# Optimization experiments

Measured on AMD Instinct MI355X. Metric: run time of the kernel, lower is better.

## Reference

```python
import jax, jax.numpy as jnp
import numpy as np

INPUT_SIZE = 256
HIDDEN_SIZE = 512
OUTPUT_SIZE = 256
SEQ_LEN = 32768


def setup_inputs() -> dict:
    key = jax.random.key(0)
    k_x, k_wx, k_wh, k_wy = jax.random.split(key, 4)
    x = jax.random.normal(k_x, (SEQ_LEN, INPUT_SIZE), dtype=jnp.float32)
    Wx = jax.random.normal(k_wx, (HIDDEN_SIZE, INPUT_SIZE), dtype=jnp.float32) * np.sqrt(2.0 / (INPUT_SIZE + HIDDEN_SIZE))
    Wh = jax.random.normal(k_wh, (HIDDEN_SIZE, HIDDEN_SIZE), dtype=jnp.float32) * np.sqrt(1.0 / HIDDEN_SIZE)
    Wy = jax.random.normal(k_wy, (OUTPUT_SIZE, HIDDEN_SIZE), dtype=jnp.float32) * np.sqrt(2.0 / (HIDDEN_SIZE + OUTPUT_SIZE))
    bh = jnp.zeros((HIDDEN_SIZE, 1), dtype=jnp.float32)
    by = jnp.zeros((OUTPUT_SIZE, 1), dtype=jnp.float32)
    return {"x": x, "Wx": Wx, "Wh": Wh, "Wy": Wy, "bh": bh, "by": by}


def reference(x, Wx, Wh, Wy, bh, by):
    # x: [T, I]; Wx: [H, I]; Wh: [H, H]; Wy: [O, H]; bh: [H,1]; by: [O,1]
    bh_v = bh[:, 0]  # [H]
    by_v = by[:, 0]  # [O]
    h0 = jnp.zeros((Wh.shape[0],), dtype=x.dtype)

    def step(h, x_t):
        # h_t = tanh(Wx @ x_t + Wh @ h_{t-1} + bh)
        h_new = jnp.tanh(Wx @ x_t + Wh @ h + bh_v)
        return h_new, h_new

    _, h_hist = jax.lax.scan(step, h0, x)  # [T, H]
    # y_t = Wy @ h_t + by, concatenated and flattened -> [T * O]
    y = h_hist @ Wy.T + by_v  # [T, O]
    return y.reshape(-1)
```

## Files before the change

kernel.cpp:

```cpp
#include <hip/hip_runtime.h>

#define SEQ 32768
#define ISZ 256
#define HSZ 512
#define OSZ 256
#define NLAUNCH 64
#define RTHREADS 512
#define SENT 0x7FAAAAAAu
#define KFAST 8
#define LATCH_T 48

typedef unsigned long long u64;
typedef _Float16 half2_t __attribute__((ext_vector_type(2)));

#if defined(__has_builtin)
#if __has_builtin(__builtin_amdgcn_fdot2)
#define HAVE_FDOT2 1
#endif
#endif

__device__ __forceinline__ float dot2f(half2_t a, half2_t b, float c) {
#ifdef HAVE_FDOT2
  return __builtin_amdgcn_fdot2(a, b, c, false);
#else
  return fmaf((float)a.x, (float)b.x, fmaf((float)a.y, (float)b.y, c));
#endif
}
__device__ __forceinline__ half2_t bch2(unsigned u) {
  return __builtin_bit_cast(half2_t, u);
}
__device__ __forceinline__ unsigned pkrtz_u(float x, float y) {
  return __builtin_bit_cast(unsigned, __builtin_amdgcn_cvt_pkrtz(x, y));
}

__global__ __launch_bounds__(256) void gemm_bt_bias(
    const float* __restrict__ A, const float* __restrict__ W,
    const float* __restrict__ bias, float* __restrict__ C,
    int M, int N, int K)
{
  __shared__ float As[32][68];
  __shared__ float Bs[32][68];
  const int tx = threadIdx.x;
  const int tn = tx & 15, tm = tx >> 4;
  const int m0 = blockIdx.x * 64, n0 = blockIdx.y * 64;
  const int kl = tx & 31;
  const int rl = tx >> 5;
  float acc[4][4] = {};

  for (int kt = 0; kt < K; kt += 32) {
#pragma unroll
    for (int i = 0; i < 8; ++i) {
      int m = rl + i * 8;
      As[kl][m] = A[(size_t)(m0 + m) * K + kt + kl];
      Bs[kl][m] = W[(size_t)(n0 + m) * K + kt + kl];
    }
    __syncthreads();
#pragma unroll
    for (int k = 0; k < 32; ++k) {
      float a[4], b[4];
#pragma unroll
      for (int i = 0; i < 4; ++i) a[i] = As[k][tm * 4 + i];
#pragma unroll
      for (int j = 0; j < 4; ++j) b[j] = Bs[k][tn * 4 + j];
#pragma unroll
      for (int i = 0; i < 4; ++i)
#pragma unroll
        for (int j = 0; j < 4; ++j)
          acc[i][j] = fmaf(a[i], b[j], acc[i][j]);
    }
    __syncthreads();
  }
#pragma unroll
  for (int i = 0; i < 4; ++i) {
    int m = m0 + tm * 4 + i;
#pragma unroll
    for (int j = 0; j < 4; ++j) {
      int n = n0 + tn * 4 + j;
      C[(size_t)m * N + n] = acc[i][j] + bias[n];
    }
  }
}

__device__ __forceinline__ float poll_sent(const float* p, unsigned sent) {
  float a, b;
  asm volatile(
      "s_waitcnt vmcnt(0)\n\t"
      "global_load_dword %0, %2, off sc0 sc1\n\t"
      "global_load_dword %1, %2, off sc0 sc1\n"
      "1:\n\t"
      "s_waitcnt vmcnt(1)\n\t"
      "v_cmp_eq_u32 vcc, %3, %0\n\t"
      "s_cbranch_vccz 3f\n\t"
      "global_load_dword %0, %2, off sc0 sc1\n\t"
      "s_waitcnt vmcnt(1)\n\t"
      "v_cmp_eq_u32 vcc, %3, %1\n\t"
      "s_cbranch_vccz 2f\n\t"
      "global_load_dword %1, %2, off sc0 sc1\n\t"
      "s_branch 1b\n"
      "2:\n\t"
      "v_mov_b32 %0, %1\n"
      "3:\n\t"
      "s_waitcnt vmcnt(0)"
      : "=&v"(a), "=&v"(b)
      : "v"(p), "v"(sent)
      : "memory", "vcc");
  return a;
}

__device__ __forceinline__ u64 load_fast(const u64* p) {
  u64 v;
  asm volatile("global_load_dwordx2 %0, %1, off sc0\n\t"
               "s_waitcnt vmcnt(0)"
               : "=v"(v) : "v"(p) : "memory");
  return v;
}
__device__ __forceinline__ void store_fast(u64* p, u64 v) {
  asm volatile("global_store_dwordx2 %0, %1, off sc0" :: "v"(p), "v"(v)
               : "memory");
}

__global__ __launch_bounds__(RTHREADS, 2) void rnn_recur(
    const float* __restrict__ P,
    const float* __restrict__ Wh,
    float* __restrict__ h_hist,
    u64* __restrict__ fring,
    int* __restrict__ elect)
{
  const int tid = threadIdx.x;
  const int w = tid >> 6;
  const int l = tid & 63;

  __shared__ float part[2][8][64];
  __shared__ int s_role;

  if (tid == 0) {
    unsigned xcc;
    asm volatile("s_getreg_b32 %0, hwreg(HW_REG_XCC_ID)" : "=s"(xcc));
    xcc &= 7u;
    int role = -1;
    int r = __hip_atomic_fetch_add(&elect[xcc], 1, __ATOMIC_RELAXED,
                                   __HIP_MEMORY_SCOPE_AGENT);
    if (r < 8) {
      if (r == 7) {
        int exp_ = -1;
        (void)__hip_atomic_compare_exchange_strong(
            &elect[8], &exp_, (int)xcc,
            __ATOMIC_RELEASE, __ATOMIC_RELAXED, __HIP_MEMORY_SCOPE_AGENT);
      }
      int wv;
      do {
        wv = __hip_atomic_load(&elect[8], __ATOMIC_ACQUIRE,
                               __HIP_MEMORY_SCOPE_AGENT);
      } while (wv < 0);
      if (wv == (int)xcc) role = r;
    }
    s_role = role;
  }
  __syncthreads();
  const int g = s_role;
  if (g < 0) return;

  const int g64 = g << 6;
  const int row = g64 + l;
  const int kbase = w << 6;

  unsigned wreg[32];
  {
    const float2* ws = (const float2*)(Wh + (size_t)row * HSZ + kbase);
#pragma unroll
    for (int j = 0; j < 32; ++j) {
      float2 f = ws[j];
      unsigned u = pkrtz_u(f.x, f.y);
      asm("" : "+v"(u));
      wreg[j] = u;
    }
  }

  const bool home = (w == g);
  float hreg = 0.f;
  float pv = home ? P[row] : 0.f;
  float pvn = 0.f;
  int fastok = 0, use_fast = 1;

  for (int t = 0; t < SEQ; ++t) {
    float vh = 0.f;
    if (home) {
      vh = hreg;
    } else if (t > 0) {
      int got = 0;
      if (use_fast) {
        const u64* fp = fring + (((size_t)g * 4 + (t & 3)) * 8 + w) * 64 + l;
        for (int k = 0; k < KFAST; ++k) {
          u64 v = load_fast(fp);
          if (__all((int)((unsigned)(v >> 32) == (unsigned)t))) {
            vh = __uint_as_float((unsigned)v);
            got = 1;
            break;
          }
        }
        if (t <= LATCH_T) {
          fastok += got;
          if (t == LATCH_T && fastok < LATCH_T - 8) use_fast = 0;
        }
      }
      if (!got)
        vh = poll_sent(h_hist + (size_t)t * HSZ + kbase + l, SENT);
    }

    float vn = __shfl_xor(vh, 1);
    unsigned hpu = pkrtz_u(vh, vn);
    float a0 = 0.f, a1 = 0.f, a2 = 0.f, a3 = 0.f;
#pragma unroll
    for (int j = 0; j < 8; ++j) {
      a0 = dot2f(bch2(wreg[4 * j + 0]),
                 bch2(__builtin_amdgcn_readlane(hpu, 8 * j + 0)), a0);
      a1 = dot2f(bch2(wreg[4 * j + 1]),
                 bch2(__builtin_amdgcn_readlane(hpu, 8 * j + 2)), a1);
      a2 = dot2f(bch2(wreg[4 * j + 2]),
                 bch2(__builtin_amdgcn_readlane(hpu, 8 * j + 4)), a2);
      a3 = dot2f(bch2(wreg[4 * j + 3]),
                 bch2(__builtin_amdgcn_readlane(hpu, 8 * j + 6)), a3);
    }
    part[t & 1][w][l] = (a0 + a1) + (a2 + a3);

    asm volatile("s_waitcnt lgkmcnt(0)\n\ts_barrier" ::: "memory");

    if (home) {
      __builtin_amdgcn_s_setprio(1);
      pvn = P[(size_t)(t + 1 < SEQ ? t + 1 : SEQ - 1) * HSZ + row];
      const int buf = t & 1;
      float p0 = part[buf][0][l], p1 = part[buf][1][l];
      float p2 = part[buf][2][l], p3 = part[buf][3][l];
      float p4 = part[buf][4][l], p5 = part[buf][5][l];
      float p6 = part[buf][6][l], p7 = part[buf][7][l];
      float s = ((p0 + p1) + (p2 + p3)) + ((p4 + p5) + (p6 + p7));
      float xv = s + pv;
      xv = fminf(fmaxf(xv, -15.f), 15.f);
      float e = __expf(2.f * xv);
      float hn = fmaf(-2.f, __builtin_amdgcn_rcpf(e + 1.f), 1.f);
      hreg = hn;
      const u64 pk = ((u64)(unsigned)(t + 1) << 32) | (u64)__float_as_uint(hn);
      const int slot = (t + 1) & 3;
#pragma unroll
      for (int j = 0; j < 8; ++j)
        store_fast(fring + (((size_t)j * 4 + slot) * 8 + g) * 64 + l, pk);
      __hip_atomic_store(&h_hist[(size_t)(t + 1) * HSZ + row], hn,
                         __ATOMIC_RELAXED, __HIP_MEMORY_SCOPE_AGENT);
      pv = pvn;
      __builtin_amdgcn_s_setprio(0);
    }
  }
}

extern "C" void kernel_launch(void* const* d_in, const int* in_sizes, int n_in,
                              void* d_out, int out_size, void* d_ws, size_t ws_size,
                              hipStream_t stream) {
  const float* x  = (const float*)d_in[0];
  const float* Wx = (const float*)d_in[1];
  const float* Wh = (const float*)d_in[2];
  const float* Wy = (const float*)d_in[3];
  const float* bh = (const float*)d_in[4];
  const float* by = (const float*)d_in[5];
  float* out = (float*)d_out;

  float* P      = (float*)d_ws;
  float* h_hist = P + (size_t)SEQ * HSZ;
  u64*   fring  = (u64*)(h_hist + (size_t)(SEQ + 1) * HSZ);
  int*   elect  = (int*)(fring + (size_t)8 * 4 * 8 * 64);

  (void)hipMemsetD32Async((hipDeviceptr_t)h_hist, (int)SENT,
                          (size_t)(SEQ + 1) * HSZ, stream);
  (void)hipMemsetAsync(h_hist, 0, HSZ * sizeof(float), stream);
  (void)hipMemsetAsync(fring, 0, (size_t)8 * 4 * 8 * 64 * sizeof(u64), stream);
  (void)hipMemsetAsync(elect, 0, 8 * sizeof(int), stream);
  (void)hipMemsetAsync(elect + 8, 0xFF, sizeof(int), stream);

  gemm_bt_bias<<<dim3(SEQ / 64, HSZ / 64), dim3(256), 0, stream>>>(
      x, Wx, bh, P, SEQ, HSZ, ISZ);

  rnn_recur<<<dim3(NLAUNCH), dim3(RTHREADS), 0, stream>>>(
      P, Wh, h_hist, fring, elect);

  gemm_bt_bias<<<dim3(SEQ / 64, OSZ / 64), dim3(256), 0, stream>>>(
      h_hist + HSZ, Wy, by, out, SEQ, OSZ, HSZ);
}
```

Baseline: 30.19 ms.

## Share single flag ring across blocks and pipeline fast-path polling loads

The per-consumer replicated fast ring (8 copies per producer) becomes a single shared ring, so each producer wave issues one store per step instead of eight. Consumers keep two outstanding polling loads in flight and alternate between them, which hides part of each load's latency. The next-step P load moves after the stores, with a partial wait. The risk is more contention, since all blocks now poll the same cache lines. The new vmcnt accounting also has to stay correct with the loads in flight.

```diff
diff --git a/kernel.cpp b/kernel.cpp
--- a/kernel.cpp
+++ b/kernel.cpp
@@ -107,12 +107,9 @@
   return a;
 }
 
-__device__ __forceinline__ u64 load_fast(const u64* p) {
-  u64 v;
-  asm volatile("global_load_dwordx2 %0, %1, off sc0\n\t"
-               "s_waitcnt vmcnt(0)"
-               : "=v"(v) : "v"(p) : "memory");
-  return v;
+__device__ __forceinline__ void issue_load(u64* v, const u64* p) {
+  asm volatile("global_load_dwordx2 %0, %1, off sc0"
+               : "=v"(*v) : "v"(p) : "memory");
 }
 __device__ __forceinline__ void store_fast(u64* p, u64 v) {
   asm volatile("global_store_dwordx2 %0, %1, off sc0" :: "v"(p), "v"(v)
@@ -189,15 +186,29 @@
     } else if (t > 0) {
       int got = 0;
       if (use_fast) {
-        const u64* fp = fring + (((size_t)g * 4 + (t & 3)) * 8 + w) * 64 + l;
+        const u64* fp = fring + (((size_t)(t & 3) * 8 + w) << 6) + l;
+        u64 v0, v1;
+        issue_load(&v0, fp);
+        issue_load(&v1, fp);
         for (int k = 0; k < KFAST; ++k) {
-          u64 v = load_fast(fp);
-          if (__all((int)((unsigned)(v >> 32) == (unsigned)t))) {
-            vh = __uint_as_float((unsigned)v);
+          asm volatile("s_waitcnt vmcnt(1)" ::: "memory");
+          __builtin_amdgcn_sched_barrier(0);
+          if (__all((int)((unsigned)(v0 >> 32) == (unsigned)t))) {
+            vh = __uint_as_float((unsigned)v0);
             got = 1;
             break;
           }
+          issue_load(&v0, fp);
+          asm volatile("s_waitcnt vmcnt(1)" ::: "memory");
+          __builtin_amdgcn_sched_barrier(0);
+          if (__all((int)((unsigned)(v1 >> 32) == (unsigned)t))) {
+            vh = __uint_as_float((unsigned)v1);
+            got = 1;
+            break;
+          }
+          issue_load(&v1, fp);
         }
+        asm volatile("s_waitcnt vmcnt(0)" ::: "memory");
         if (t <= LATCH_T) {
           fastok += got;
           if (t == LATCH_T && fastok < LATCH_T - 8) use_fast = 0;
@@ -227,7 +238,6 @@
 
     if (home) {
       __builtin_amdgcn_s_setprio(1);
-      pvn = P[(size_t)(t + 1 < SEQ ? t + 1 : SEQ - 1) * HSZ + row];
       const int buf = t & 1;
       float p0 = part[buf][0][l], p1 = part[buf][1][l];
       float p2 = part[buf][2][l], p3 = part[buf][3][l];
@@ -240,12 +250,11 @@
       float hn = fmaf(-2.f, __builtin_amdgcn_rcpf(e + 1.f), 1.f);
       hreg = hn;
       const u64 pk = ((u64)(unsigned)(t + 1) << 32) | (u64)__float_as_uint(hn);
-      const int slot = (t + 1) & 3;
-#pragma unroll
-      for (int j = 0; j < 8; ++j)
-        store_fast(fring + (((size_t)j * 4 + slot) * 8 + g) * 64 + l, pk);
+      store_fast(fring + (((size_t)((t + 1) & 3) * 8 + g) << 6) + l, pk);
       __hip_atomic_store(&h_hist[(size_t)(t + 1) * HSZ + row], hn,
                          __ATOMIC_RELAXED, __HIP_MEMORY_SCOPE_AGENT);
+      asm volatile("s_waitcnt vmcnt(1)" ::: "memory");
+      pvn = P[(size_t)(t + 1 < SEQ ? t + 1 : SEQ - 1) * HSZ + row];
       pv = pvn;
       __builtin_amdgcn_s_setprio(0);
     }
@@ -266,12 +275,12 @@
   float* P      = (float*)d_ws;
   float* h_hist = P + (size_t)SEQ * HSZ;
   u64*   fring  = (u64*)(h_hist + (size_t)(SEQ + 1) * HSZ);
-  int*   elect  = (int*)(fring + (size_t)8 * 4 * 8 * 64);
+  int*   elect  = (int*)(fring + (size_t)4 * 8 * 64);
 
   (void)hipMemsetD32Async((hipDeviceptr_t)h_hist, (int)SENT,
                           (size_t)(SEQ + 1) * HSZ, stream);
   (void)hipMemsetAsync(h_hist, 0, HSZ * sizeof(float), stream);
-  (void)hipMemsetAsync(fring, 0, (size_t)8 * 4 * 8 * 64 * sizeof(u64), stream);
+  (void)hipMemsetAsync(fring, 0, (size_t)4 * 8 * 64 * sizeof(u64), stream);
   (void)hipMemsetAsync(elect, 0, 8 * sizeof(int), stream);
   (void)hipMemsetAsync(elect + 8, 0xFF, sizeof(int), stream);
 
```

New measurement: 33.80 ms. 1.12x slower.
